# Kernel tuning notes

Hardware: AMD Instinct MI355X
Metric: run time of the kernel (lower is better)

The kernel has to match this reference:

```python
import jax, jax.numpy as jnp
import numpy as np

N, K, D_IN, D_OUT = 50000, 16, 256, 256
LN_EPS = 1e-5


def setup_inputs() -> dict:
    key = jax.random.key(0)
    k1, k2, k3, k4 = jax.random.split(key, 4)
    features = jax.random.normal(k1, (N, D_IN), dtype=jnp.float32)
    neighbors = jax.random.randint(k2, (N, K), 0, N, dtype=jnp.int64)
    importance_weights = jax.random.uniform(k3, (N, K), dtype=jnp.float32)
    # Linear(in_channels, out_channels): weight stored as [D_IN, D_OUT] for x @ W + b
    W = jax.random.normal(k4, (D_IN, D_OUT), dtype=jnp.float32) * (1.0 / np.sqrt(D_IN))
    b = jnp.zeros((D_OUT,), dtype=jnp.float32)
    gamma = jnp.ones((D_OUT,), dtype=jnp.float32)
    beta = jnp.zeros((D_OUT,), dtype=jnp.float32)
    return {"features": features, "neighbors": neighbors,
            "importance_weights": importance_weights,
            "W": W, "b": b, "gamma": gamma, "beta": beta}


def reference(features, neighbors, importance_weights, W, b, gamma, beta):
    # Gather neighbor features: [N, K, D_IN]
    neigh_feats = features[neighbors]
    # Linear transform: [N, K, D_OUT]
    transformed = jnp.einsum('nkd,df->nkf', neigh_feats, W) + b
    # Normalize importance weights per node; zero-sum fallback = uniform mean
    wsum = jnp.sum(importance_weights, axis=-1, keepdims=True)  # [N, 1]
    norm_w = jnp.where(wsum == 0.0,
                       jnp.full_like(importance_weights, 1.0 / K),
                       importance_weights / jnp.where(wsum == 0.0, 1.0, wsum))
    # Importance-weighted sum over neighbors: [N, D_OUT]
    agg = jnp.einsum('nkf,nk->nf', transformed, norm_w)
    # LayerNorm over feature dim (torch: biased variance, eps=1e-5)
    mean = jnp.mean(agg, axis=-1, keepdims=True)
    var = jnp.mean((agg - mean) ** 2, axis=-1, keepdims=True)
    out = (agg - mean) * jax.lax.rsqrt(var + LN_EPS) * gamma + beta
    return out
```

## Files before the change

kernel.cpp:

```cpp
#include <hip/hip_runtime.h>


#define NN   50000
#define KNB  16
#define D    256

typedef __attribute__((ext_vector_type(8))) short short8;
typedef __attribute__((ext_vector_type(4))) float f32x4;

static __device__ __forceinline__ unsigned short f2bf(float x) {
    unsigned int u = __float_as_uint(x);
    return (unsigned short)((u + 0x7FFFu + ((u >> 16) & 1u)) >> 16);
}
static __device__ __forceinline__ float bf2f(unsigned short h) {
    return __uint_as_float((unsigned int)h << 16);
}

__global__ __launch_bounds__(256) void convert_w(const float* __restrict__ Wm,
                                                 unsigned short* __restrict__ wtp) {
    const int g    = blockIdx.x * 256 + threadIdx.x;
    const int lane = g & 63;
    const int kb32 = (g >> 6) & 7;
    const int c    = g >> 9;
    const int n    = c * 16 + (lane & 15);
    const int k0   = kb32 * 32 + (lane >> 4) * 8;
    short8 v;
    #pragma unroll
    for (int j = 0; j < 8; ++j) v[j] = (short)f2bf(Wm[(size_t)(k0 + j) * D + n]);
    *(short8*)(wtp + (size_t)g * 8) = v;
}

__global__ __launch_bounds__(256) void convert_feat(const float* __restrict__ feat,
                                                    unsigned short* __restrict__ featb) {
    const size_t g = (size_t)blockIdx.x * 256 + threadIdx.x;
    const float4 a = *(const float4*)(feat + g * 8);
    const float4 b = *(const float4*)(feat + g * 8 + 4);
    short8 o;
    o[0] = (short)f2bf(a.x); o[1] = (short)f2bf(a.y);
    o[2] = (short)f2bf(a.z); o[3] = (short)f2bf(a.w);
    o[4] = (short)f2bf(b.x); o[5] = (short)f2bf(b.y);
    o[6] = (short)f2bf(b.z); o[7] = (short)f2bf(b.w);
    *(short8*)(featb + g * 8) = o;
}

__global__ __launch_bounds__(256, 8) void pool_b(const unsigned short* __restrict__ featb,
                                                 const int*   __restrict__ nbr,
                                                 const float* __restrict__ iw,
                                                 unsigned short* __restrict__ aggb) {
    const int  t    = threadIdx.x;
    const int  lane = t & 63;
    const int  wq   = t >> 6;
    const long n    = (long)blockIdx.x * 4 + wq;

    float ws = 0.f;
    #pragma unroll
    for (int k = 0; k < KNB; ++k) ws += iw[n * KNB + k];
    const bool  zs  = (ws == 0.f);
    const float inv = zs ? (1.f / KNB) : (1.f / ws);

    float4 p = make_float4(0.f, 0.f, 0.f, 0.f);
    #pragma unroll 1
    for (int kb = 0; kb < KNB; kb += 8) {
        int   idx[8];
        float w[8];
        #pragma unroll
        for (int k = 0; k < 8; ++k) {
            idx[k] = nbr[n * KNB + kb + k];
            w[k]   = iw [n * KNB + kb + k];
        }
        #pragma unroll
        for (int k = 0; k < 8; ++k) {
            const float   wk = zs ? inv : (w[k] * inv);
            const ushort4 u  = *(const ushort4*)(featb + (size_t)idx[k] * D + lane * 4);
            p.x += wk * bf2f(u.x); p.y += wk * bf2f(u.y);
            p.z += wk * bf2f(u.z); p.w += wk * bf2f(u.w);
        }
    }
    ushort4 o;
    o.x = f2bf(p.x); o.y = f2bf(p.y); o.z = f2bf(p.z); o.w = f2bf(p.w);
    *(ushort4*)(aggb + (size_t)n * 512 + lane * 4) = o;
}

__global__ __launch_bounds__(256, 8) void pool_f(const float* __restrict__ feat,
                                                 const int*   __restrict__ nbr,
                                                 const float* __restrict__ iw,
                                                 unsigned short* __restrict__ aggb) {
    const int  t    = threadIdx.x;
    const int  lane = t & 63;
    const int  wq   = t >> 6;
    const long n    = (long)blockIdx.x * 4 + wq;
    float ws = 0.f;
    #pragma unroll
    for (int k = 0; k < KNB; ++k) ws += iw[n * KNB + k];
    const bool  zs  = (ws == 0.f);
    const float inv = zs ? (1.f / KNB) : (1.f / ws);
    float4 p = make_float4(0.f, 0.f, 0.f, 0.f);
    #pragma unroll 1
    for (int kb = 0; kb < KNB; kb += 8) {
        int idx[8]; float w[8];
        #pragma unroll
        for (int k = 0; k < 8; ++k) { idx[k] = nbr[n*KNB+kb+k]; w[k] = iw[n*KNB+kb+k]; }
        #pragma unroll
        for (int k = 0; k < 8; ++k) {
            const float  wk = zs ? inv : (w[k] * inv);
            const float4 f  = *(const float4*)(feat + (size_t)idx[k] * D + lane * 4);
            p.x += wk*f.x; p.y += wk*f.y; p.z += wk*f.z; p.w += wk*f.w;
        }
    }
    ushort4 o;
    o.x = f2bf(p.x); o.y = f2bf(p.y); o.z = f2bf(p.z); o.w = f2bf(p.w);
    *(ushort4*)(aggb + (size_t)n * 512 + lane * 4) = o;
}

__global__ __launch_bounds__(256, 2) void gemm_ln(const unsigned short* __restrict__ aggb,
                                                  const unsigned short* __restrict__ wtp,
                                                  const float* __restrict__ bias,
                                                  const float* __restrict__ gamma,
                                                  const float* __restrict__ beta,
                                                  float* __restrict__ out) {
    __shared__ float sO[64][257];

    const int t       = threadIdx.x;
    const int lane    = t & 63;
    const int wq      = t >> 6;
    const int quad    = lane >> 4;
    const int l15     = lane & 15;
    const int rowbase = blockIdx.x * 64 + wq * 16;

    const int arow = min(rowbase + l15, NN - 1);
    const unsigned short* aptr = aggb + (size_t)arow * 512 + quad * 8;
    const short8* wv = (const short8*)wtp;

    f32x4 acc[16];
    #pragma unroll
    for (int c = 0; c < 16; ++c) acc[c] = (f32x4){0.f, 0.f, 0.f, 0.f};

    #pragma unroll
    for (int kb32 = 0; kb32 < 8; ++kb32) {
        const short8 a = *(const short8*)(aptr + kb32 * 32);
        #pragma unroll
        for (int c = 0; c < 16; ++c) {
            const short8 b = wv[(size_t)(c * 8 + kb32) * 64 + lane];
            acc[c] = __builtin_amdgcn_mfma_f32_16x16x32_bf16(a, b, acc[c], 0, 0, 0);
        }
    }

    float bv[16], gv[16], btv[16];
    #pragma unroll
    for (int c = 0; c < 16; ++c) {
        bv[c]  = bias [c * 16 + l15];
        gv[c]  = gamma[c * 16 + l15];
        btv[c] = beta [c * 16 + l15];
    }
    #pragma unroll
    for (int j = 0; j < 4; ++j) {
        float s = 0.f, sq = 0.f;
        #pragma unroll
        for (int c = 0; c < 16; ++c) {
            const float v = acc[c][j] + bv[c];
            s += v; sq += v * v;
        }
        #pragma unroll
        for (int off = 1; off < 16; off <<= 1) {
            s  += __shfl_xor(s,  off, 64);
            sq += __shfl_xor(sq, off, 64);
        }
        const float mean = s * (1.f / D);
        const float var  = sq * (1.f / D) - mean * mean;
        const float rstd = rsqrtf(var + 1e-5f);
        const int   lrow = wq * 16 + quad * 4 + j;
        #pragma unroll
        for (int c = 0; c < 16; ++c) {
            const float v = acc[c][j] + bv[c];
            sO[lrow][c * 16 + l15] = (v - mean) * rstd * gv[c] + btv[c];
        }
    }
    __syncthreads();

    #pragma unroll
    for (int p = 0; p < 16; ++p) {
        const int row = p * 4 + wq;
        const int r   = blockIdx.x * 64 + row;
        if (r < NN)
            *(float4*)(out + (size_t)r * D + lane * 4) = *(float4*)&sO[row][lane * 4];
    }
}

extern "C" void kernel_launch(void* const* d_in, const int* in_sizes, int n_in,
                              void* d_out, int out_size, void* d_ws, size_t ws_size,
                              hipStream_t stream) {
    const float* feat = (const float*)d_in[0];
    const int*   nbr  = (const int*)d_in[1];
    const float* iw   = (const float*)d_in[2];
    const float* Wm   = (const float*)d_in[3];
    const float* b    = (const float*)d_in[4];
    const float* g    = (const float*)d_in[5];
    const float* be   = (const float*)d_in[6];
    float*       out  = (float*)d_out;

    unsigned short* wtp   = (unsigned short*)d_ws;
    unsigned short* featb = (unsigned short*)((char*)d_ws + 131072);
    unsigned short* aggb  = (unsigned short*)d_out;

    const size_t need = 131072 + (size_t)NN * D * 2;

    convert_w<<<dim3(32), dim3(256), 0, stream>>>(Wm, wtp);
    if (ws_size >= need) {
        convert_feat<<<dim3(6250),    dim3(256), 0, stream>>>(feat, featb);
        pool_b      <<<dim3(NN / 4),  dim3(256), 0, stream>>>(featb, nbr, iw, aggb);
    } else {
        pool_f      <<<dim3(NN / 4),  dim3(256), 0, stream>>>(feat, nbr, iw, aggb);
    }
    gemm_ln<<<dim3((NN + 63) / 64), dim3(256), 0, stream>>>(aggb, wtp, b, g, be, out);
}
```

Measured before the change: 190.9 us.

## Widen pooling gathers to 16-byte loads and double gemm rows per wave

In pool_b, each node is now handled by 32 lanes that each gather 8 bf16 values with one 16-byte load, so a 256-thread block covers 8 nodes instead of 4. Neighbor indices and weights are loaded once as int4/float4 vectors instead of scalar reads. In gemm_ln, each wave computes 32 rows with two accumulator sets that share each W fragment, which halves W traffic per row. The LDS staging and block barrier are dropped, so LayerNorm output is written straight to global memory in 64-byte strided chunks, at the cost of less coalesced stores and higher register pressure.

```diff
diff --git a/kernel.cpp b/kernel.cpp
--- a/kernel.cpp
+++ b/kernel.cpp
@@ -43,42 +43,45 @@
     *(short8*)(featb + g * 8) = o;
 }
 
-__global__ __launch_bounds__(256, 8) void pool_b(const unsigned short* __restrict__ featb,
+__global__ __launch_bounds__(256, 6) void pool_b(const unsigned short* __restrict__ featb,
                                                  const int*   __restrict__ nbr,
                                                  const float* __restrict__ iw,
                                                  unsigned short* __restrict__ aggb) {
-    const int  t    = threadIdx.x;
-    const int  lane = t & 63;
-    const int  wq   = t >> 6;
-    const long n    = (long)blockIdx.x * 4 + wq;
-
+    const int  t   = threadIdx.x;
+    const int  l31 = t & 31;
+    const long n   = (long)blockIdx.x * 8 + (t >> 5);
+
+    float w[KNB];
+    int   idx[KNB];
+    #pragma unroll
+    for (int q = 0; q < 4; ++q) {
+        const float4 w4 = *(const float4*)(iw  + n * KNB + q * 4);
+        const int4   i4 = *(const int4*)  (nbr + n * KNB + q * 4);
+        w[q*4+0] = w4.x; w[q*4+1] = w4.y; w[q*4+2] = w4.z; w[q*4+3] = w4.w;
+        idx[q*4+0] = i4.x; idx[q*4+1] = i4.y; idx[q*4+2] = i4.z; idx[q*4+3] = i4.w;
+    }
     float ws = 0.f;
     #pragma unroll
-    for (int k = 0; k < KNB; ++k) ws += iw[n * KNB + k];
+    for (int k = 0; k < KNB; ++k) ws += w[k];
     const bool  zs  = (ws == 0.f);
     const float inv = zs ? (1.f / KNB) : (1.f / ws);
 
-    float4 p = make_float4(0.f, 0.f, 0.f, 0.f);
+    float p[8] = {0.f, 0.f, 0.f, 0.f, 0.f, 0.f, 0.f, 0.f};
     #pragma unroll 1
     for (int kb = 0; kb < KNB; kb += 8) {
-        int   idx[8];
-        float w[8];
         #pragma unroll
         for (int k = 0; k < 8; ++k) {
-            idx[k] = nbr[n * KNB + kb + k];
-            w[k]   = iw [n * KNB + kb + k];
-        }
-        #pragma unroll
-        for (int k = 0; k < 8; ++k) {
-            const float   wk = zs ? inv : (w[k] * inv);
-            const ushort4 u  = *(const ushort4*)(featb + (size_t)idx[k] * D + lane * 4);
-            p.x += wk * bf2f(u.x); p.y += wk * bf2f(u.y);
-            p.z += wk * bf2f(u.z); p.w += wk * bf2f(u.w);
-        }
-    }
-    ushort4 o;
-    o.x = f2bf(p.x); o.y = f2bf(p.y); o.z = f2bf(p.z); o.w = f2bf(p.w);
-    *(ushort4*)(aggb + (size_t)n * 512 + lane * 4) = o;
+            const float  wk = zs ? inv : (w[kb + k] * inv);
+            const short8 u  = *(const short8*)(featb + (size_t)idx[kb + k] * D + l31 * 8);
+            #pragma unroll
+            for (int e = 0; e < 8; ++e)
+                p[e] += wk * bf2f((unsigned short)u[e]);
+        }
+    }
+    short8 o;
+    #pragma unroll
+    for (int e = 0; e < 8; ++e) o[e] = (short)f2bf(p[e]);
+    *(short8*)(aggb + (size_t)n * 512 + l31 * 8) = o;
 }
 
 __global__ __launch_bounds__(256, 8) void pool_f(const float* __restrict__ feat,
@@ -118,30 +121,35 @@
                                                   const float* __restrict__ gamma,
                                                   const float* __restrict__ beta,
                                                   float* __restrict__ out) {
-    __shared__ float sO[64][257];
-
     const int t       = threadIdx.x;
     const int lane    = t & 63;
     const int wq      = t >> 6;
     const int quad    = lane >> 4;
     const int l15     = lane & 15;
-    const int rowbase = blockIdx.x * 64 + wq * 16;
-
-    const int arow = min(rowbase + l15, NN - 1);
-    const unsigned short* aptr = aggb + (size_t)arow * 512 + quad * 8;
+    const int rowbase = blockIdx.x * 128 + wq * 32;
+
+    const int ar0 = min(rowbase +      l15, NN - 1);
+    const int ar1 = min(rowbase + 16 + l15, NN - 1);
+    const unsigned short* ap0 = aggb + (size_t)ar0 * 512 + quad * 8;
+    const unsigned short* ap1 = aggb + (size_t)ar1 * 512 + quad * 8;
     const short8* wv = (const short8*)wtp;
 
-    f32x4 acc[16];
-    #pragma unroll
-    for (int c = 0; c < 16; ++c) acc[c] = (f32x4){0.f, 0.f, 0.f, 0.f};
-
-    #pragma unroll
-    for (int kb32 = 0; kb32 < 8; ++kb32) {
-        const short8 a = *(const short8*)(aptr + kb32 * 32);
+    f32x4 acc0[16], acc1[16];
+    #pragma unroll
+    for (int c = 0; c < 16; ++c) {
+        acc0[c] = (f32x4){0.f, 0.f, 0.f, 0.f};
+        acc1[c] = (f32x4){0.f, 0.f, 0.f, 0.f};
+    }
+
+    #pragma unroll
+    for (int kb = 0; kb < 8; ++kb) {
+        const short8 a0 = *(const short8*)(ap0 + kb * 32);
+        const short8 a1 = *(const short8*)(ap1 + kb * 32);
         #pragma unroll
         for (int c = 0; c < 16; ++c) {
-            const short8 b = wv[(size_t)(c * 8 + kb32) * 64 + lane];
-            acc[c] = __builtin_amdgcn_mfma_f32_16x16x32_bf16(a, b, acc[c], 0, 0, 0);
+            const short8 b = wv[(size_t)(c * 8 + kb) * 64 + lane];
+            acc0[c] = __builtin_amdgcn_mfma_f32_16x16x32_bf16(a0, b, acc0[c], 0, 0, 0);
+            acc1[c] = __builtin_amdgcn_mfma_f32_16x16x32_bf16(a1, b, acc1[c], 0, 0, 0);
         }
     }
 
@@ -153,36 +161,32 @@
         btv[c] = beta [c * 16 + l15];
     }
     #pragma unroll
-    for (int j = 0; j < 4; ++j) {
-        float s = 0.f, sq = 0.f;
-        #pragma unroll
-        for (int c = 0; c < 16; ++c) {
-            const float v = acc[c][j] + bv[c];
-            s += v; sq += v * v;
-        }
-        #pragma unroll
-        for (int off = 1; off < 16; off <<= 1) {
-            s  += __shfl_xor(s,  off, 64);
-            sq += __shfl_xor(sq, off, 64);
-        }
-        const float mean = s * (1.f / D);
-        const float var  = sq * (1.f / D) - mean * mean;
-        const float rstd = rsqrtf(var + 1e-5f);
-        const int   lrow = wq * 16 + quad * 4 + j;
-        #pragma unroll
-        for (int c = 0; c < 16; ++c) {
-            const float v = acc[c][j] + bv[c];
-            sO[lrow][c * 16 + l15] = (v - mean) * rstd * gv[c] + btv[c];
-        }
-    }
-    __syncthreads();
-
-    #pragma unroll
-    for (int p = 0; p < 16; ++p) {
-        const int row = p * 4 + wq;
-        const int r   = blockIdx.x * 64 + row;
-        if (r < NN)
-            *(float4*)(out + (size_t)r * D + lane * 4) = *(float4*)&sO[row][lane * 4];
+    for (int m = 0; m < 2; ++m) {
+        const f32x4* acc = m ? acc1 : acc0;
+        #pragma unroll
+        for (int j = 0; j < 4; ++j) {
+            float s = 0.f, sq = 0.f;
+            #pragma unroll
+            for (int c = 0; c < 16; ++c) {
+                const float v = acc[c][j] + bv[c];
+                s += v; sq += v * v;
+            }
+            #pragma unroll
+            for (int off = 1; off < 16; off <<= 1) {
+                s  += __shfl_xor(s,  off, 64);
+                sq += __shfl_xor(sq, off, 64);
+            }
+            const float mean = s * (1.f / D);
+            const float var  = sq * (1.f / D) - mean * mean;
+            const float rstd = rsqrtf(var + 1e-5f);
+            const int   r    = rowbase + m * 16 + quad * 4 + j;
+            if (r < NN) {
+                float* op = out + (size_t)r * D + l15;
+                #pragma unroll
+                for (int c = 0; c < 16; ++c)
+                    op[c * 16] = (acc[c][j] + bv[c] - mean) * rstd * gv[c] + btv[c];
+            }
+        }
     }
 }
 
@@ -206,10 +210,10 @@
 
     convert_w<<<dim3(32), dim3(256), 0, stream>>>(Wm, wtp);
     if (ws_size >= need) {
-        convert_feat<<<dim3(6250),    dim3(256), 0, stream>>>(feat, featb);
-        pool_b      <<<dim3(NN / 4),  dim3(256), 0, stream>>>(featb, nbr, iw, aggb);
+        convert_feat<<<dim3(6250),   dim3(256), 0, stream>>>(feat, featb);
+        pool_b      <<<dim3(NN / 8), dim3(256), 0, stream>>>(featb, nbr, iw, aggb);
     } else {
-        pool_f      <<<dim3(NN / 4),  dim3(256), 0, stream>>>(feat, nbr, iw, aggb);
-    }
-    gemm_ln<<<dim3((NN + 63) / 64), dim3(256), 0, stream>>>(aggb, wtp, b, g, be, out);
-}
+        pool_f      <<<dim3(NN / 4), dim3(256), 0, stream>>>(feat, nbr, iw, aggb);
+    }
+    gemm_ln<<<dim3((NN + 127) / 128), dim3(256), 0, stream>>>(aggb, wtp, b, g, be, out);
+}
```

After: 210.6 us. 10.3% more time.
